# Performance work log

Hardware: AMD Instinct MI355X
Metric: run time of the kernel (lower is better)

The kernel has to match this reference:

```python
import jax, jax.numpy as jnp
import numpy as np

DT = 0.1
B_SZ = 8192
T_HIST = 20
LEN_PRED = 30
FEAT = 32
N_LAYERS = 3
# state transition for constant-acceleration model (matches self.F in torch)
F_MAT = np.array([[1.0, DT, DT * DT / 2], [0.0, 1.0, DT], [0.0, 0.0, 1.0]], dtype=np.float32)


def setup_inputs() -> dict:
    key = jax.random.key(0)
    ks = jax.random.split(key, 16)
    # random-walk trajectories as history observations
    hist = jnp.cumsum(jax.random.normal(ks[0], (B_SZ, T_HIST, 2), jnp.float32) * 0.5, axis=1)
    k_lin = 1.0 / np.sqrt(FEAT)
    k_in = 1.0 / np.sqrt(24)

    def u(k, shape, scale):
        return jax.random.uniform(k, shape, jnp.float32, -scale, scale)

    return {
        "hist": hist,
        "max_accel_x": jnp.ones((1,), jnp.float32) * 10.0,
        "max_accel_y": jnp.ones((1,), jnp.float32) * 20.0,
        "velocity_std_x": jnp.ones((1,), jnp.float32) * 10.0,
        "acceleration_std_x": jnp.ones((1,), jnp.float32) * 10.0,
        "R_x_": jnp.array([0.0448], jnp.float32),
        "R_y_": jnp.array([0.001], jnp.float32),
        "G_x": jnp.array([0.0059, 0.2981, 0.0393], jnp.float32),
        "G_y": jnp.array([0.0059, 0.2981, 0.0393], jnp.float32) / 5.0,
        "Win_W": u(ks[1], (FEAT, 24), k_in),
        "Win_b": u(ks[2], (FEAT,), k_in),
        "enc_Wih": u(ks[3], (N_LAYERS, 4 * FEAT, FEAT), k_lin),
        "enc_Whh": u(ks[4], (N_LAYERS, 4 * FEAT, FEAT), k_lin),
        "enc_bih": u(ks[5], (N_LAYERS, 4 * FEAT), k_lin),
        "enc_bhh": u(ks[6], (N_LAYERS, 4 * FEAT), k_lin),
        "dec_Wih": u(ks[7], (N_LAYERS, 4 * FEAT, FEAT), k_lin),
        "dec_Whh": u(ks[8], (N_LAYERS, 4 * FEAT, FEAT), k_lin),
        "dec_bih": u(ks[9], (N_LAYERS, 4 * FEAT), k_lin),
        "dec_bhh": u(ks[10], (N_LAYERS, 4 * FEAT), k_lin),
        "Wout_W": u(ks[11], (4, FEAT), k_lin),
        "Wout_b": u(ks[12], (4,), k_lin),
        "len_pred": LEN_PRED,
    }


def reference(hist, max_accel_x, max_accel_y, velocity_std_x, acceleration_std_x,
              R_x_, R_y_, G_x, G_y, Win_W, Win_b,
              enc_Wih, enc_Whh, enc_bih, enc_bhh,
              dec_Wih, dec_Whh, dec_bih, dec_bhh,
              Wout_W, Wout_b, len_pred):
    B = hist.shape[0]
    F = jnp.asarray(F_MAT)
    R_x = R_x_[0] * R_x_[0]
    R_y = R_y_[0] * R_y_[0]
    Z_x = hist[:, :, 0]
    Z_y = hist[:, :, 1]

    def lstm(x, h, c, Wih, Whh, bih, bhh):
        g = x @ Wih.T + bih + h @ Whh.T + bhh
        i, f, gg, o = jnp.split(g, 4, axis=1)
        c = jax.nn.sigmoid(f) * c + jax.nn.sigmoid(i) * jnp.tanh(gg)
        h = jax.nn.sigmoid(o) * jnp.tanh(c)
        return h, c

    def stack(XP, h, c, Wih, Whh, bih, bhh):
        x = jnp.tanh(XP @ Win_W.T + Win_b)
        hs, cs = [], []
        for j in range(N_LAYERS):
            hj, cj = lstm(x, h[j], c[j], Wih[j], Whh[j], bih[j], bhh[j])
            hs.append(hj)
            cs.append(cj)
            x = cj  # torch code feeds the fresh CELL state to the next layer
        return jnp.stack(hs), jnp.stack(cs)

    def kpred(X, P, Q):
        return X @ F.T, jnp.einsum('ij,bjk,lk->bil', F, P, F) + Q

    def kupdate(X, P, z, R):
        y = z - X[:, 0]                      # innovation (H picks component 0)
        S = P[:, 0, 0] + R                   # innovation covariance (scalar)
        K = P[:, :, 0] / S[:, None]          # Kalman gain (B,3)
        return X + y[:, None] * K, P - K[:, :, None] * P[:, 0:1, :]

    def kinit(z0):
        # torch always calls _kalman_init with is_x=True (default), so both
        # axes use R_x / velocity_std_x / acceleration_std_x
        X = jnp.zeros((B, 3), hist.dtype).at[:, 0].set(z0)
        d = jnp.stack([R_x, velocity_std_x[0] ** 2, acceleration_std_x[0] ** 2])
        P = jnp.zeros((B, 3, 3), hist.dtype).at[:, jnp.arange(3), jnp.arange(3)].set(d)
        return X, P

    Qx_e = jnp.outer(G_x * max_accel_x[0], G_x * max_accel_x[0])
    Qy_e = jnp.outer(G_y * max_accel_y[0], G_y * max_accel_y[0])

    Xx, Px = kinit(Z_x[:, 0])
    Xy, Py = kinit(Z_y[:, 0])
    h = jnp.zeros((N_LAYERS, B, FEAT), hist.dtype)
    c = jnp.zeros_like(h)

    def enc_step(carry, zs):
        Xx, Px, Xy, Py, h, c = carry
        zx, zy = zs
        XP = jnp.concatenate([Xx, Xy, Px.reshape(B, 9), Py.reshape(B, 9)], 1)
        h, c = stack(XP, h, c, enc_Wih, enc_Whh, enc_bih, enc_bhh)
        Xx, Px = kpred(Xx, Px, Qx_e)
        Xy, Py = kpred(Xy, Py, Qy_e)
        Xx, Px = kupdate(Xx, Px, zx, R_x)
        Xy, Py = kupdate(Xy, Py, zy, R_y)
        return (Xx, Px, Xy, Py, h, c), None

    carry, _ = jax.lax.scan(enc_step, (Xx, Px, Xy, Py, h, c),
                            (Z_x[:, 1:].T, Z_y[:, 1:].T))

    oxx = jnp.outer(G_x, G_x)
    oyy = jnp.outer(G_y, G_y)

    def dec_step(carry, _):
        Xx, Px, Xy, Py, h, c = carry
        XP = jnp.concatenate([Xx, Xy, Px.reshape(B, 9), Py.reshape(B, 9)], 1)
        h, c = stack(XP, h, c, dec_Wih, dec_Whh, dec_bih, dec_bhh)
        pred = c[-1] @ Wout_W.T + Wout_b  # (B,4): [u_x, u_y, std_x, std_y]
        Xx = Xx.at[:, 2].set(DT * pred[:, 0])  # X[:,2] = B*u
        Xy = Xy.at[:, 2].set(DT * pred[:, 1])
        Qx = (pred[:, 2] ** 2)[:, None, None] * oxx
        Qy = (pred[:, 3] ** 2)[:, None, None] * oyy
        Xx, Px = kpred(Xx, Px, Qx)
        Xy, Py = kpred(Xy, Py, Qy)
        out = jnp.stack([Xx[:, 0], Xy[:, 0],
                         jnp.sqrt(Px[:, 0, 0]), jnp.sqrt(Py[:, 0, 0]),
                         jnp.zeros(B, hist.dtype)], axis=1)  # (B,5)
        return (Xx, Px, Xy, Py, h, c), out

    carry, ys = jax.lax.scan(dec_step, carry, None, length=len_pred)
    return jnp.transpose(ys, (1, 0, 2))  # (B, len_pred, 5)
```

## Files before the change

kernel.cpp:

```cpp
#include <hip/hip_runtime.h>
#include <math.h>

#define DT   0.1f
#define HDT  0.005f
#define T_HIST 20
#define LEN_PRED 30

typedef __attribute__((ext_vector_type(8))) short bfrag8;
typedef __attribute__((ext_vector_type(4))) short short4v;
typedef __attribute__((ext_vector_type(4))) float f32x4;

#define WS_FRAG   0u
#define WS_WIN    98304u
#define WS_WOUT   100352u
#define WS_BIAS   101376u
#define WS_WINB   104448u
#define WS_WOUTB  104576u

static __device__ __forceinline__ unsigned short f2bf(float x) {
    union { float f; unsigned int u; } v; v.f = x;
    unsigned int r = v.u + 0x7fffu + ((v.u >> 16) & 1u);
    return (unsigned short)(r >> 16);
}

__global__ void prep_kernel(const float* __restrict__ Win_W, const float* __restrict__ Win_b,
                            const float* __restrict__ eWih, const float* __restrict__ eWhh,
                            const float* __restrict__ ebih, const float* __restrict__ ebhh,
                            const float* __restrict__ dWih, const float* __restrict__ dWhh,
                            const float* __restrict__ dbih, const float* __restrict__ dbhh,
                            const float* __restrict__ Wout_W, const float* __restrict__ Wout_b,
                            char* __restrict__ ws)
{
    int i = blockIdx.x * blockDim.x + threadIdx.x;
    if (i < 49152) {
        int lin = i >> 9, within = i & 511;
        int lane = within >> 3, j = within & 7;
        int c = lin & 1, g_t = (lin >> 1) & 7;
        int pl = lin >> 4;
        int l = pl % 3, phase = pl / 3;
        int m = lane & 15, q2 = lane >> 4;
        int row = g_t * 16 + m, k = q2 * 8 + j;
        const float* W = (c == 0) ? (phase ? dWih : eWih) : (phase ? dWhh : eWhh);
        ((unsigned short*)(ws + WS_FRAG))[i] = f2bf(W[l * 4096 + row * 32 + k]);
    } else if (i < 50176) {
        int i2 = i - 49152;
        int wv = i2 >> 9, within = i2 & 511;
        int lane = within >> 3, j = within & 7;
        int m = lane & 15, q2 = lane >> 4;
        int row = wv * 16 + m, k = q2 * 8 + j;
        float v = (k < 24) ? Win_W[row * 24 + k] : 0.f;
        ((unsigned short*)(ws + WS_WIN))[i2] = f2bf(v);
    } else if (i < 50688) {
        int i3 = i - 50176;
        int lane = i3 >> 3, j = i3 & 7;
        int m = lane & 15, q2 = lane >> 4;
        int k = q2 * 8 + j;
        float v = (m < 4) ? Wout_W[m * 32 + k] : 0.f;
        ((unsigned short*)(ws + WS_WOUT))[i3] = f2bf(v);
    } else if (i < 51456) {
        int b = i - 50688;
        int phase = b / 384, rem = b % 384;
        int l = rem / 128, row = rem % 128;
        const float* bi = phase ? dbih : ebih;
        const float* bh = phase ? dbhh : ebhh;
        ((float*)(ws + WS_BIAS))[b] = bi[l * 128 + row] + bh[l * 128 + row];
    } else if (i < 51488) {
        int b = i - 51456;
        ((float*)(ws + WS_WINB))[b] = Win_b[b];
    } else if (i < 51492) {
        int b = i - 51488;
        ((float*)(ws + WS_WOUTB))[b] = Wout_b[b];
    }
}

__launch_bounds__(128, 1)
__global__ void kalman_lstm_kernel(const float* __restrict__ hist,
                                   const float* __restrict__ max_ax, const float* __restrict__ max_ay,
                                   const float* __restrict__ vstd, const float* __restrict__ astd,
                                   const float* __restrict__ Rx_, const float* __restrict__ Ry_,
                                   const float* __restrict__ Gx, const float* __restrict__ Gy,
                                   const char* __restrict__ ws, float* __restrict__ out)
{
    __shared__ __align__(16) unsigned short xp[16][40];
    __shared__ __align__(16) unsigned short xin[4][16][40];
    __shared__ __align__(16) unsigned short hbuf[2][3][16][40];
    __shared__ __align__(16) float bias_lds[2][3][128];

    const int tid = threadIdx.x;
    const int w = tid >> 6;
    const int lane = tid & 63;
    const int q = lane >> 4;
    const int m = lane & 15;
    const int base = blockIdx.x * 16;
    const int b_elem = base + m;

    bfrag8 fragL[2][3][4][2];
    const bfrag8* fragp = (const bfrag8*)(ws + WS_FRAG);
#pragma unroll
    for (int ph = 0; ph < 2; ++ph)
#pragma unroll
        for (int l = 0; l < 3; ++l)
#pragma unroll
            for (int kd = 0; kd < 4; ++kd)
#pragma unroll
                for (int c = 0; c < 2; ++c) {
                    int g_t = w + 2 * kd;
                    int fi = ((ph * 3 + l) * 8 + g_t) * 2 + c;
                    fragL[ph][l][kd][c] = fragp[fi * 64 + lane];
                }
    bfrag8 winF  = ((const bfrag8*)(ws + WS_WIN))[w * 64 + lane];
    bfrag8 woutF = ((const bfrag8*)(ws + WS_WOUT))[lane];
    f32x4 winB   = *(const f32x4*)(ws + WS_WINB + (unsigned)((w * 16 + q * 4) * 4));
    f32x4 woutB  = *(const f32x4*)(ws + WS_WOUTB);

    for (int idx = tid; idx < 768; idx += 128)
        ((float*)bias_lds)[idx] = ((const float*)(ws + WS_BIAS))[idx];
    for (int idx = tid; idx < 16 * 40; idx += 128) (&xp[0][0])[idx] = 0;
    for (int idx = tid; idx < 4 * 16 * 40; idx += 128) (&xin[0][0][0])[idx] = 0;
    for (int idx = tid; idx < 2 * 3 * 16 * 40; idx += 128) (&hbuf[0][0][0][0])[idx] = 0;

    const float rx = Rx_[0] * Rx_[0], ry = Ry_[0] * Ry_[0];
    const float Rch = w ? ry : rx;
    const float v2 = vstd[0] * vstd[0], a2 = astd[0] * astd[0];
    float g0, g1, g2, ge0, ge1, ge2;
    if (w == 0) { g0 = Gx[0]; g1 = Gx[1]; g2 = Gx[2]; float s = max_ax[0]; ge0 = g0*s; ge1 = g1*s; ge2 = g2*s; }
    else        { g0 = Gy[0]; g1 = Gy[1]; g2 = Gy[2]; float s = max_ay[0]; ge0 = g0*s; ge1 = g1*s; ge2 = g2*s; }

    float X0 = hist[b_elem * (T_HIST * 2) + w], X1 = 0.f, X2 = 0.f;
    float P00 = rx, P01 = 0.f, P02 = 0.f, P11 = v2, P12 = 0.f, P22 = a2;

    float creg[3][4];
#pragma unroll
    for (int l = 0; l < 3; ++l)
#pragma unroll
        for (int r = 0; r < 4; ++r) creg[l][r] = 0.f;

    auto write_xp = [&]() {
        if (q == 0) {
            int o = w * 3;
            xp[m][o + 0] = f2bf(X0); xp[m][o + 1] = f2bf(X1); xp[m][o + 2] = f2bf(X2);
            int pb = 6 + w * 9;
            xp[m][pb + 0] = f2bf(P00); xp[m][pb + 1] = f2bf(P01); xp[m][pb + 2] = f2bf(P02);
            xp[m][pb + 3] = f2bf(P01); xp[m][pb + 4] = f2bf(P11); xp[m][pb + 5] = f2bf(P12);
            xp[m][pb + 6] = f2bf(P02); xp[m][pb + 7] = f2bf(P12); xp[m][pb + 8] = f2bf(P22);
        }
    };

    auto sig = [](float z) { return __builtin_amdgcn_rcpf(1.f + __expf(-z)); };
    auto th  = [](float z) { return fmaf(-2.f, __builtin_amdgcn_rcpf(__expf(2.f * z) + 1.f), 1.f); };

    auto kpred = [&](float Q00, float Q01, float Q02, float Q11, float Q12, float Q22) {
        X0 = X0 + DT * X1 + HDT * X2;
        X1 = X1 + DT * X2;
        float M00 = P00 + DT * P01 + HDT * P02;
        float M01 = P01 + DT * P11 + HDT * P12;
        float M02 = P02 + DT * P12 + HDT * P22;
        float M11 = P11 + DT * P12;
        float M12 = P12 + DT * P22;
        float M22 = P22;
        P00 = M00 + DT * M01 + HDT * M02 + Q00;
        P01 = M01 + DT * M02 + Q01;
        P02 = M02 + Q02;
        P11 = M11 + DT * M12 + Q11;
        P12 = M12 + Q12;
        P22 = M22 + Q22;
    };

    const f32x4 zero4 = {0.f, 0.f, 0.f, 0.f};

    auto stack = [&](int ph, int p) {
        bfrag8 bxp = *(const bfrag8*)&xp[m][q * 8];
        f32x4 aw = __builtin_amdgcn_mfma_f32_16x16x32_bf16(winF, bxp, zero4, 0, 0, 0);
        {
            union { short4v v; unsigned short s[4]; } u;
#pragma unroll
            for (int r = 0; r < 4; ++r) u.s[r] = f2bf(th(aw[r] + winB[r]));
            *(short4v*)&xin[0][m][w * 16 + q * 4] = u.v;
        }
        __syncthreads();
#pragma unroll
        for (int l = 0; l < 3; ++l) {
            bfrag8 bx = *(const bfrag8*)&xin[l][m][q * 8];
            bfrag8 bh = *(const bfrag8*)&hbuf[p][l][m][q * 8];
            f32x4 acc[4];
#pragma unroll
            for (int kd = 0; kd < 4; ++kd) {
                f32x4 t0 = __builtin_amdgcn_mfma_f32_16x16x32_bf16(fragL[ph][l][kd][0], bx, zero4, 0, 0, 0);
                acc[kd]  = __builtin_amdgcn_mfma_f32_16x16x32_bf16(fragL[ph][l][kd][1], bh, t0, 0, 0, 0);
            }
            f32x4 bb[4];
#pragma unroll
            for (int kd = 0; kd < 4; ++kd)
                bb[kd] = *(const f32x4*)&bias_lds[ph][l][16 * (w + 2 * kd) + 4 * q];
            union { short4v v; unsigned short s[4]; } hc, cc;
#pragma unroll
            for (int r = 0; r < 4; ++r) {
                float iv = sig(acc[0][r] + bb[0][r]);
                float fv = sig(acc[1][r] + bb[1][r]);
                float gv = th (acc[2][r] + bb[2][r]);
                float ov = sig(acc[3][r] + bb[3][r]);
                float cn = fmaf(fv, creg[l][r], iv * gv);
                float hn = ov * th(cn);
                creg[l][r] = cn;
                hc.s[r] = f2bf(hn);
                cc.s[r] = f2bf(cn);
            }
            *(short4v*)&hbuf[p ^ 1][l][m][w * 16 + q * 4] = hc.v;
            *(short4v*)&xin[l + 1][m][w * 16 + q * 4] = cc.v;
            __syncthreads();
        }
    };

    __syncthreads();
    write_xp();
    int parity = 0;

    for (int t = 0; t < T_HIST - 1; ++t) {
        __syncthreads();
        float z = hist[b_elem * (T_HIST * 2) + (t + 1) * 2 + w];
        stack(0, parity);
        kpred(ge0 * ge0, ge0 * ge1, ge0 * ge2, ge1 * ge1, ge1 * ge2, ge2 * ge2);
        float y = z - X0;
        float S = P00 + Rch;
        float Sinv = 1.0f / S;
        float K0 = P00 * Sinv, K1 = P01 * Sinv, K2 = P02 * Sinv;
        X0 += y * K0; X1 += y * K1; X2 += y * K2;
        float p00 = P00, p01 = P01, p02 = P02;
        P00 = p00 - K0 * p00;
        P01 = p01 - K0 * p01;
        P02 = p02 - K0 * p02;
        P11 = P11 - K1 * p01;
        P12 = P12 - K1 * p02;
        P22 = P22 - K2 * p02;
        write_xp();
        parity ^= 1;
    }

    for (int t = 0; t < LEN_PRED; ++t) {
        __syncthreads();
        stack(1, parity);
        bfrag8 bc2 = *(const bfrag8*)&xin[3][m][q * 8];
        f32x4 ap = __builtin_amdgcn_mfma_f32_16x16x32_bf16(woutF, bc2, zero4, 0, 0, 0);
        float pe = (w == 0) ? (ap[0] + woutB[0]) : (ap[1] + woutB[1]);
        float qe = (w == 0) ? (ap[2] + woutB[2]) : (ap[3] + woutB[3]);
        X2 = DT * pe;
        float qs = qe * qe;
        kpred(qs * g0 * g0, qs * g0 * g1, qs * g0 * g2, qs * g1 * g1, qs * g1 * g2, qs * g2 * g2);
        if (q == 0) {
            float* o = out + (size_t)b_elem * (LEN_PRED * 5) + t * 5;
            if (w == 0) { o[0] = X0; o[2] = sqrtf(P00); }
            else        { o[1] = X0; o[3] = sqrtf(P00); o[4] = 0.f; }
        }
        write_xp();
        parity ^= 1;
    }
}

extern "C" void kernel_launch(void* const* d_in, const int* in_sizes, int n_in,
                              void* d_out, int out_size, void* d_ws, size_t ws_size,
                              hipStream_t stream)
{
    const float* hist  = (const float*)d_in[0];
    const float* maxax = (const float*)d_in[1];
    const float* maxay = (const float*)d_in[2];
    const float* vstd  = (const float*)d_in[3];
    const float* astd  = (const float*)d_in[4];
    const float* Rx    = (const float*)d_in[5];
    const float* Ry    = (const float*)d_in[6];
    const float* Gx    = (const float*)d_in[7];
    const float* Gy    = (const float*)d_in[8];
    const float* WinW  = (const float*)d_in[9];
    const float* Winb  = (const float*)d_in[10];
    const float* eWih  = (const float*)d_in[11];
    const float* eWhh  = (const float*)d_in[12];
    const float* ebih  = (const float*)d_in[13];
    const float* ebhh  = (const float*)d_in[14];
    const float* dWih  = (const float*)d_in[15];
    const float* dWhh  = (const float*)d_in[16];
    const float* dbih  = (const float*)d_in[17];
    const float* dbhh  = (const float*)d_in[18];
    const float* WoutW = (const float*)d_in[19];
    const float* Woutb = (const float*)d_in[20];
    char* ws = (char*)d_ws;
    float* out = (float*)d_out;

    prep_kernel<<<202, 256, 0, stream>>>(WinW, Winb, eWih, eWhh, ebih, ebhh,
                                         dWih, dWhh, dbih, dbhh, WoutW, Woutb, ws);
    kalman_lstm_kernel<<<512, 128, 0, stream>>>(hist, maxax, maxay, vstd, astd,
                                                Rx, Ry, Gx, Gy, ws, out);
}
```

Baseline: 202.1 us.

## Use four waves per block with LDS gate exchange and drop prep kernel

```diff
diff --git a/kernel.cpp b/kernel.cpp
--- a/kernel.cpp
+++ b/kernel.cpp
@@ -9,13 +9,7 @@
 typedef __attribute__((ext_vector_type(8))) short bfrag8;
 typedef __attribute__((ext_vector_type(4))) short short4v;
 typedef __attribute__((ext_vector_type(4))) float f32x4;
-
-#define WS_FRAG   0u
-#define WS_WIN    98304u
-#define WS_WOUT   100352u
-#define WS_BIAS   101376u
-#define WS_WINB   104448u
-#define WS_WOUTB  104576u
+typedef __attribute__((ext_vector_type(2))) float f32x2;
 
 static __device__ __forceinline__ unsigned short f2bf(float x) {
     union { float f; unsigned int u; } v; v.f = x;
@@ -23,123 +17,106 @@
     return (unsigned short)(r >> 16);
 }
 
-__global__ void prep_kernel(const float* __restrict__ Win_W, const float* __restrict__ Win_b,
-                            const float* __restrict__ eWih, const float* __restrict__ eWhh,
-                            const float* __restrict__ ebih, const float* __restrict__ ebhh,
-                            const float* __restrict__ dWih, const float* __restrict__ dWhh,
-                            const float* __restrict__ dbih, const float* __restrict__ dbhh,
-                            const float* __restrict__ Wout_W, const float* __restrict__ Wout_b,
-                            char* __restrict__ ws)
-{
-    int i = blockIdx.x * blockDim.x + threadIdx.x;
-    if (i < 49152) {
-        int lin = i >> 9, within = i & 511;
-        int lane = within >> 3, j = within & 7;
-        int c = lin & 1, g_t = (lin >> 1) & 7;
-        int pl = lin >> 4;
-        int l = pl % 3, phase = pl / 3;
-        int m = lane & 15, q2 = lane >> 4;
-        int row = g_t * 16 + m, k = q2 * 8 + j;
-        const float* W = (c == 0) ? (phase ? dWih : eWih) : (phase ? dWhh : eWhh);
-        ((unsigned short*)(ws + WS_FRAG))[i] = f2bf(W[l * 4096 + row * 32 + k]);
-    } else if (i < 50176) {
-        int i2 = i - 49152;
-        int wv = i2 >> 9, within = i2 & 511;
-        int lane = within >> 3, j = within & 7;
-        int m = lane & 15, q2 = lane >> 4;
-        int row = wv * 16 + m, k = q2 * 8 + j;
-        float v = (k < 24) ? Win_W[row * 24 + k] : 0.f;
-        ((unsigned short*)(ws + WS_WIN))[i2] = f2bf(v);
-    } else if (i < 50688) {
-        int i3 = i - 50176;
-        int lane = i3 >> 3, j = i3 & 7;
-        int m = lane & 15, q2 = lane >> 4;
-        int k = q2 * 8 + j;
-        float v = (m < 4) ? Wout_W[m * 32 + k] : 0.f;
-        ((unsigned short*)(ws + WS_WOUT))[i3] = f2bf(v);
-    } else if (i < 51456) {
-        int b = i - 50688;
-        int phase = b / 384, rem = b % 384;
-        int l = rem / 128, row = rem % 128;
-        const float* bi = phase ? dbih : ebih;
-        const float* bh = phase ? dbhh : ebhh;
-        ((float*)(ws + WS_BIAS))[b] = bi[l * 128 + row] + bh[l * 128 + row];
-    } else if (i < 51488) {
-        int b = i - 51456;
-        ((float*)(ws + WS_WINB))[b] = Win_b[b];
-    } else if (i < 51492) {
-        int b = i - 51488;
-        ((float*)(ws + WS_WOUTB))[b] = Wout_b[b];
-    }
-}
-
-__launch_bounds__(128, 1)
+__launch_bounds__(256, 1)
 __global__ void kalman_lstm_kernel(const float* __restrict__ hist,
                                    const float* __restrict__ max_ax, const float* __restrict__ max_ay,
                                    const float* __restrict__ vstd, const float* __restrict__ astd,
                                    const float* __restrict__ Rx_, const float* __restrict__ Ry_,
                                    const float* __restrict__ Gx, const float* __restrict__ Gy,
-                                   const char* __restrict__ ws, float* __restrict__ out)
+                                   const float* __restrict__ Win_W, const float* __restrict__ Win_b,
+                                   const float* __restrict__ eWih, const float* __restrict__ eWhh,
+                                   const float* __restrict__ ebih, const float* __restrict__ ebhh,
+                                   const float* __restrict__ dWih, const float* __restrict__ dWhh,
+                                   const float* __restrict__ dbih, const float* __restrict__ dbhh,
+                                   const float* __restrict__ Wout_W, const float* __restrict__ Wout_b,
+                                   float* __restrict__ out)
 {
     __shared__ __align__(16) unsigned short xp[16][40];
     __shared__ __align__(16) unsigned short xin[4][16][40];
     __shared__ __align__(16) unsigned short hbuf[2][3][16][40];
     __shared__ __align__(16) float bias_lds[2][3][128];
-
-    const int tid = threadIdx.x;
-    const int w = tid >> 6;
+    __shared__ __align__(16) float pre[4][32][18];
+
+    const int tid  = threadIdx.x;
+    const int wv   = tid >> 6;
     const int lane = tid & 63;
-    const int q = lane >> 4;
-    const int m = lane & 15;
+    const int q    = lane >> 4;
+    const int m    = lane & 15;
     const int base = blockIdx.x * 16;
     const int b_elem = base + m;
 
-    bfrag8 fragL[2][3][4][2];
-    const bfrag8* fragp = (const bfrag8*)(ws + WS_FRAG);
+    bfrag8 fragL[2][3][2][2];
 #pragma unroll
     for (int ph = 0; ph < 2; ++ph)
 #pragma unroll
         for (int l = 0; l < 3; ++l)
 #pragma unroll
-            for (int kd = 0; kd < 4; ++kd)
+            for (int t = 0; t < 2; ++t)
 #pragma unroll
                 for (int c = 0; c < 2; ++c) {
-                    int g_t = w + 2 * kd;
-                    int fi = ((ph * 3 + l) * 8 + g_t) * 2 + c;
-                    fragL[ph][l][kd][c] = fragp[fi * 64 + lane];
+                    const float* W = (c == 0) ? (ph ? dWih : eWih) : (ph ? dWhh : eWhh);
+                    int row = wv * 32 + t * 16 + m;
+                    union { bfrag8 v; unsigned short s[8]; } u;
+#pragma unroll
+                    for (int j = 0; j < 8; ++j)
+                        u.s[j] = f2bf(W[l * 4096 + row * 32 + q * 8 + j]);
+                    fragL[ph][l][t][c] = u.v;
                 }
-    bfrag8 winF  = ((const bfrag8*)(ws + WS_WIN))[w * 64 + lane];
-    bfrag8 woutF = ((const bfrag8*)(ws + WS_WOUT))[lane];
-    f32x4 winB   = *(const f32x4*)(ws + WS_WINB + (unsigned)((w * 16 + q * 4) * 4));
-    f32x4 woutB  = *(const f32x4*)(ws + WS_WOUTB);
-
-    for (int idx = tid; idx < 768; idx += 128)
-        ((float*)bias_lds)[idx] = ((const float*)(ws + WS_BIAS))[idx];
-    for (int idx = tid; idx < 16 * 40; idx += 128) (&xp[0][0])[idx] = 0;
-    for (int idx = tid; idx < 4 * 16 * 40; idx += 128) (&xin[0][0][0])[idx] = 0;
-    for (int idx = tid; idx < 2 * 3 * 16 * 40; idx += 128) (&hbuf[0][0][0][0])[idx] = 0;
-
-    const float rx = Rx_[0] * Rx_[0], ry = Ry_[0] * Ry_[0];
-    const float Rch = w ? ry : rx;
-    const float v2 = vstd[0] * vstd[0], a2 = astd[0] * astd[0];
-    float g0, g1, g2, ge0, ge1, ge2;
-    if (w == 0) { g0 = Gx[0]; g1 = Gx[1]; g2 = Gx[2]; float s = max_ax[0]; ge0 = g0*s; ge1 = g1*s; ge2 = g2*s; }
-    else        { g0 = Gy[0]; g1 = Gy[1]; g2 = Gy[2]; float s = max_ay[0]; ge0 = g0*s; ge1 = g1*s; ge2 = g2*s; }
-
-    float X0 = hist[b_elem * (T_HIST * 2) + w], X1 = 0.f, X2 = 0.f;
-    float P00 = rx, P01 = 0.f, P02 = 0.f, P11 = v2, P12 = 0.f, P22 = a2;
-
-    float creg[3][4];
-#pragma unroll
-    for (int l = 0; l < 3; ++l)
-#pragma unroll
-        for (int r = 0; r < 4; ++r) creg[l][r] = 0.f;
+
+    bfrag8 winF = {}, woutF = {};
+    f32x4 winB = {0.f, 0.f, 0.f, 0.f}, woutB = {0.f, 0.f, 0.f, 0.f};
+    if (wv < 2) {
+        union { bfrag8 v; unsigned short s[8]; } u;
+#pragma unroll
+        for (int j = 0; j < 8; ++j) {
+            int k = q * 8 + j;
+            u.s[j] = (k < 24) ? f2bf(Win_W[(wv * 16 + m) * 24 + k]) : 0;
+        }
+        winF = u.v;
+#pragma unroll
+        for (int j = 0; j < 8; ++j)
+            u.s[j] = (m < 4) ? f2bf(Wout_W[m * 32 + q * 8 + j]) : 0;
+        woutF = u.v;
+#pragma unroll
+        for (int r = 0; r < 4; ++r) winB[r] = Win_b[wv * 16 + q * 4 + r];
+#pragma unroll
+        for (int r = 0; r < 4; ++r) woutB[r] = Wout_b[r];
+    }
+
+    for (int idx = tid; idx < 768; idx += 256) {
+        int ph = idx / 384, rem = idx - ph * 384;
+        int l = rem >> 7, row = rem & 127;
+        const float* bi = ph ? dbih : ebih;
+        const float* bh = ph ? dbhh : ebhh;
+        ((float*)bias_lds)[idx] = bi[l * 128 + row] + bh[l * 128 + row];
+    }
+    for (int idx = tid; idx < 16 * 40; idx += 256) (&xp[0][0])[idx] = 0;
+    for (int idx = tid; idx < 4 * 16 * 40; idx += 256) (&xin[0][0][0])[idx] = 0;
+    for (int idx = tid; idx < 2 * 3 * 16 * 40; idx += 256) (&hbuf[0][0][0][0])[idx] = 0;
+
+    float g0 = 0.f, g1 = 0.f, g2 = 0.f, ge0 = 0.f, ge1 = 0.f, ge2 = 0.f;
+    float Rch = 0.f, X0 = 0.f, X1 = 0.f, X2 = 0.f;
+    float P00 = 0.f, P01 = 0.f, P02 = 0.f, P11 = 0.f, P12 = 0.f, P22 = 0.f;
+    if (wv < 2) {
+        const float rx = Rx_[0] * Rx_[0], ry = Ry_[0] * Ry_[0];
+        Rch = wv ? ry : rx;
+        if (wv == 0) { g0 = Gx[0]; g1 = Gx[1]; g2 = Gx[2]; float s = max_ax[0]; ge0 = g0*s; ge1 = g1*s; ge2 = g2*s; }
+        else         { g0 = Gy[0]; g1 = Gy[1]; g2 = Gy[2]; float s = max_ay[0]; ge0 = g0*s; ge1 = g1*s; ge2 = g2*s; }
+        X0 = hist[b_elem * (T_HIST * 2) + wv];
+        P00 = Rch; P11 = vstd[0] * vstd[0]; P22 = astd[0] * astd[0];
+    }
+
+    const int feat = tid >> 3;
+    const int e0 = (tid & 7) * 2;
+    float creg[3][2];
+#pragma unroll
+    for (int l = 0; l < 3; ++l) { creg[l][0] = 0.f; creg[l][1] = 0.f; }
 
     auto write_xp = [&]() {
-        if (q == 0) {
-            int o = w * 3;
+        if (wv < 2 && q == 0) {
+            int o = wv * 3;
             xp[m][o + 0] = f2bf(X0); xp[m][o + 1] = f2bf(X1); xp[m][o + 2] = f2bf(X2);
-            int pb = 6 + w * 9;
+            int pb = 6 + wv * 9;
             xp[m][pb + 0] = f2bf(P00); xp[m][pb + 1] = f2bf(P01); xp[m][pb + 2] = f2bf(P02);
             xp[m][pb + 3] = f2bf(P01); xp[m][pb + 4] = f2bf(P11); xp[m][pb + 5] = f2bf(P12);
             xp[m][pb + 6] = f2bf(P02); xp[m][pb + 7] = f2bf(P12); xp[m][pb + 8] = f2bf(P22);
@@ -169,44 +146,46 @@
     const f32x4 zero4 = {0.f, 0.f, 0.f, 0.f};
 
     auto stack = [&](int ph, int p) {
-        bfrag8 bxp = *(const bfrag8*)&xp[m][q * 8];
-        f32x4 aw = __builtin_amdgcn_mfma_f32_16x16x32_bf16(winF, bxp, zero4, 0, 0, 0);
-        {
+        if (wv < 2) {
+            bfrag8 bxp = *(const bfrag8*)&xp[m][q * 8];
+            f32x4 aw = __builtin_amdgcn_mfma_f32_16x16x32_bf16(winF, bxp, zero4, 0, 0, 0);
             union { short4v v; unsigned short s[4]; } u;
 #pragma unroll
             for (int r = 0; r < 4; ++r) u.s[r] = f2bf(th(aw[r] + winB[r]));
-            *(short4v*)&xin[0][m][w * 16 + q * 4] = u.v;
+            *(short4v*)&xin[0][m][wv * 16 + q * 4] = u.v;
         }
         __syncthreads();
 #pragma unroll
         for (int l = 0; l < 3; ++l) {
             bfrag8 bx = *(const bfrag8*)&xin[l][m][q * 8];
             bfrag8 bh = *(const bfrag8*)&hbuf[p][l][m][q * 8];
-            f32x4 acc[4];
-#pragma unroll
-            for (int kd = 0; kd < 4; ++kd) {
-                f32x4 t0 = __builtin_amdgcn_mfma_f32_16x16x32_bf16(fragL[ph][l][kd][0], bx, zero4, 0, 0, 0);
-                acc[kd]  = __builtin_amdgcn_mfma_f32_16x16x32_bf16(fragL[ph][l][kd][1], bh, t0, 0, 0, 0);
+            f32x4 a0 = __builtin_amdgcn_mfma_f32_16x16x32_bf16(fragL[ph][l][0][0], bx, zero4, 0, 0, 0);
+            a0        = __builtin_amdgcn_mfma_f32_16x16x32_bf16(fragL[ph][l][0][1], bh, a0, 0, 0, 0);
+            f32x4 a1 = __builtin_amdgcn_mfma_f32_16x16x32_bf16(fragL[ph][l][1][0], bx, zero4, 0, 0, 0);
+            a1        = __builtin_amdgcn_mfma_f32_16x16x32_bf16(fragL[ph][l][1][1], bh, a1, 0, 0, 0);
+            f32x4 bb0 = *(const f32x4*)&bias_lds[ph][l][wv * 32 + q * 4];
+            f32x4 bb1 = *(const f32x4*)&bias_lds[ph][l][wv * 32 + 16 + q * 4];
+#pragma unroll
+            for (int r = 0; r < 4; ++r) pre[wv][q * 4 + r][m] = a0[r] + bb0[r];
+#pragma unroll
+            for (int r = 0; r < 4; ++r) pre[wv][16 + q * 4 + r][m] = a1[r] + bb1[r];
+            __syncthreads();
+            f32x2 gi = *(const f32x2*)&pre[0][feat][e0];
+            f32x2 gf = *(const f32x2*)&pre[1][feat][e0];
+            f32x2 gg = *(const f32x2*)&pre[2][feat][e0];
+            f32x2 go = *(const f32x2*)&pre[3][feat][e0];
+#pragma unroll
+            for (int j = 0; j < 2; ++j) {
+                float iv = sig(gi[j]);
+                float fv = sig(gf[j]);
+                float gvv = th(gg[j]);
+                float ov = sig(go[j]);
+                float cn = fmaf(fv, creg[l][j], iv * gvv);
+                float hn = ov * th(cn);
+                creg[l][j] = cn;
+                xin[l + 1][e0 + j][feat] = f2bf(cn);
+                hbuf[p ^ 1][l][e0 + j][feat] = f2bf(hn);
             }
-            f32x4 bb[4];
-#pragma unroll
-            for (int kd = 0; kd < 4; ++kd)
-                bb[kd] = *(const f32x4*)&bias_lds[ph][l][16 * (w + 2 * kd) + 4 * q];
-            union { short4v v; unsigned short s[4]; } hc, cc;
-#pragma unroll
-            for (int r = 0; r < 4; ++r) {
-                float iv = sig(acc[0][r] + bb[0][r]);
-                float fv = sig(acc[1][r] + bb[1][r]);
-                float gv = th (acc[2][r] + bb[2][r]);
-                float ov = sig(acc[3][r] + bb[3][r]);
-                float cn = fmaf(fv, creg[l][r], iv * gv);
-                float hn = ov * th(cn);
-                creg[l][r] = cn;
-                hc.s[r] = f2bf(hn);
-                cc.s[r] = f2bf(cn);
-            }
-            *(short4v*)&hbuf[p ^ 1][l][m][w * 16 + q * 4] = hc.v;
-            *(short4v*)&xin[l + 1][m][w * 16 + q * 4] = cc.v;
             __syncthreads();
         }
     };
@@ -217,41 +196,45 @@
 
     for (int t = 0; t < T_HIST - 1; ++t) {
         __syncthreads();
-        float z = hist[b_elem * (T_HIST * 2) + (t + 1) * 2 + w];
+        float z = 0.f;
+        if (wv < 2) z = hist[b_elem * (T_HIST * 2) + (t + 1) * 2 + wv];
         stack(0, parity);
-        kpred(ge0 * ge0, ge0 * ge1, ge0 * ge2, ge1 * ge1, ge1 * ge2, ge2 * ge2);
-        float y = z - X0;
-        float S = P00 + Rch;
-        float Sinv = 1.0f / S;
-        float K0 = P00 * Sinv, K1 = P01 * Sinv, K2 = P02 * Sinv;
-        X0 += y * K0; X1 += y * K1; X2 += y * K2;
-        float p00 = P00, p01 = P01, p02 = P02;
-        P00 = p00 - K0 * p00;
-        P01 = p01 - K0 * p01;
-        P02 = p02 - K0 * p02;
-        P11 = P11 - K1 * p01;
-        P12 = P12 - K1 * p02;
-        P22 = P22 - K2 * p02;
-        write_xp();
+        if (wv < 2) {
+            kpred(ge0 * ge0, ge0 * ge1, ge0 * ge2, ge1 * ge1, ge1 * ge2, ge2 * ge2);
+            float y = z - X0;
+            float Sinv = 1.0f / (P00 + Rch);
+            float K0 = P00 * Sinv, K1 = P01 * Sinv, K2 = P02 * Sinv;
+            X0 += y * K0; X1 += y * K1; X2 += y * K2;
+            float p00 = P00, p01 = P01, p02 = P02;
+            P00 = p00 - K0 * p00;
+            P01 = p01 - K0 * p01;
+            P02 = p02 - K0 * p02;
+            P11 = P11 - K1 * p01;
+            P12 = P12 - K1 * p02;
+            P22 = P22 - K2 * p02;
+            write_xp();
+        }
         parity ^= 1;
     }
 
     for (int t = 0; t < LEN_PRED; ++t) {
         __syncthreads();
         stack(1, parity);
-        bfrag8 bc2 = *(const bfrag8*)&xin[3][m][q * 8];
-        f32x4 ap = __builtin_amdgcn_mfma_f32_16x16x32_bf16(woutF, bc2, zero4, 0, 0, 0);
-        float pe = (w == 0) ? (ap[0] + woutB[0]) : (ap[1] + woutB[1]);
-        float qe = (w == 0) ? (ap[2] + woutB[2]) : (ap[3] + woutB[3]);
-        X2 = DT * pe;
-        float qs = qe * qe;
-        kpred(qs * g0 * g0, qs * g0 * g1, qs * g0 * g2, qs * g1 * g1, qs * g1 * g2, qs * g2 * g2);
-        if (q == 0) {
-            float* o = out + (size_t)b_elem * (LEN_PRED * 5) + t * 5;
-            if (w == 0) { o[0] = X0; o[2] = sqrtf(P00); }
-            else        { o[1] = X0; o[3] = sqrtf(P00); o[4] = 0.f; }
-        }
-        write_xp();
+        if (wv < 2) {
+            bfrag8 bc2 = *(const bfrag8*)&xin[3][m][q * 8];
+            f32x4 ap = __builtin_amdgcn_mfma_f32_16x16x32_bf16(woutF, bc2, zero4, 0, 0, 0);
+            float pe = (wv == 0) ? (ap[0] + woutB[0]) : (ap[1] + woutB[1]);
+            float qe = (wv == 0) ? (ap[2] + woutB[2]) : (ap[3] + woutB[3]);
+            X2 = DT * pe;
+            float qs = qe * qe;
+            kpred(qs * g0 * g0, qs * g0 * g1, qs * g0 * g2, qs * g1 * g1, qs * g1 * g2, qs * g2 * g2);
+            if (q == 0) {
+                float* o = out + (size_t)b_elem * (LEN_PRED * 5) + t * 5;
+                if (wv == 0) { o[0] = X0; o[2] = sqrtf(P00); }
+                else         { o[1] = X0; o[3] = sqrtf(P00); o[4] = 0.f; }
+            }
+            write_xp();
+        }
         parity ^= 1;
     }
 }
@@ -281,11 +264,11 @@
     const float* dbhh  = (const float*)d_in[18];
     const float* WoutW = (const float*)d_in[19];
     const float* Woutb = (const float*)d_in[20];
-    char* ws = (char*)d_ws;
     float* out = (float*)d_out;
 
-    prep_kernel<<<202, 256, 0, stream>>>(WinW, Winb, eWih, eWhh, ebih, ebhh,
-                                         dWih, dWhh, dbih, dbhh, WoutW, Woutb, ws);
-    kalman_lstm_kernel<<<512, 128, 0, stream>>>(hist, maxax, maxay, vstd, astd,
-                                                Rx, Ry, Gx, Gy, ws, out);
+    kalman_lstm_kernel<<<512, 256, 0, stream>>>(hist, maxax, maxay, vstd, astd,
+                                                Rx, Ry, Gx, Gy,
+                                                WinW, Winb, eWih, eWhh, ebih, ebhh,
+                                                dWih, dWhh, dbih, dbhh, WoutW, Woutb,
+                                                out);
 }
```

New measurement: 303.7 us. 50.3% more time.
